# Kernel optimization log

Hardware: AMD Instinct MI355X
Metric: run time of the kernel (lower is better)

The kernel has to match this reference:

```python
import jax, jax.numpy as jnp
import numpy as np
from jax import lax

D, H, DH, F, K, L, N = 512, 8, 64, 2048, 31, 512, 16
EPS = 1e-5

def layer_norm(x, g, b):
    m = x.mean(-1, keepdims=True)
    v = ((x - m) ** 2).mean(-1, keepdims=True)
    return (x - m) / jnp.sqrt(v + EPS) * g + b

def swish(x):
    return x * jax.nn.sigmoid(x)

def ffn(x, w1, b1, w2, b2):
    return swish(x @ w1.T + b1) @ w2.T + b2

def rel_shift(x):
    # x: (N,H,T,2T-1) -> (N,H,T,T); out[...,i,j] = x[...,i, T-1-i+j]
    T = x.shape[2]
    rows = jnp.arange(T)[:, None]
    cols = (T - 1) - rows + jnp.arange(T)[None, :]
    return x[:, :, rows, cols]

def rel_attn(x, pos_emb, in_w, in_b, out_w, out_b, pos_w, bu, bv):
    Lq, Nb, E = x.shape
    qkv = x @ in_w.T + in_b  # (L,N,3E)
    q, k, v = jnp.split(qkv, 3, axis=-1)
    q = q.reshape(Lq, Nb, H, DH).transpose(1, 2, 0, 3)  # (N,H,L,DH)
    k = k.reshape(Lq, Nb, H, DH).transpose(1, 2, 0, 3)
    v = v.reshape(Lq, Nb, H, DH).transpose(1, 2, 0, 3)
    p = (pos_emb[0] @ pos_w.T).reshape(-1, H, DH).transpose(1, 0, 2)  # (H,2L-1,DH)
    scaling = DH ** -0.5
    q_u = q + bu[None, :, None, :]
    q_v = q + bv[None, :, None, :]
    matrix_ac = jnp.einsum('nhld,nhsd->nhls', q_u, k)        # (N,H,L,L)
    matrix_bd = jnp.einsum('nhld,hmd->nhlm', q_v, p)         # (N,H,L,2L-1)
    matrix_bd = rel_shift(matrix_bd)                         # (N,H,L,L)
    attn = jax.nn.softmax((matrix_ac + matrix_bd) * scaling, axis=-1)
    out = jnp.einsum('nhls,nhsd->nhld', attn, v)
    out = out.transpose(2, 0, 1, 3).reshape(Lq, Nb, E)
    return out @ out_w.T + out_b

def conv_module(x, pw1_w, pw1_b, dw_w, dw_b, g, b, mean, var, pw2_w, pw2_b):
    # x: (L,N,C) -> (N,C,L)
    y = x.transpose(1, 2, 0)
    y = jnp.einsum('ncl,oc->nol', y, pw1_w) + pw1_b[None, :, None]
    a, gate = jnp.split(y, 2, axis=1)
    y = a * jax.nn.sigmoid(gate)  # GLU over channel dim
    pad = (K - 1) // 2
    y = lax.conv_general_dilated(y, dw_w[:, None, :], (1,), [(pad, pad)],
                                 feature_group_count=D,
                                 dimension_numbers=('NCH', 'OIH', 'NCH'))
    y = y + dw_b[None, :, None]
    # BatchNorm1d in eval mode with running stats
    y = (y - mean[None, :, None]) / jnp.sqrt(var[None, :, None] + EPS)
    y = y * g[None, :, None] + b[None, :, None]
    y = swish(y)
    y = jnp.einsum('ncl,oc->nol', y, pw2_w) + pw2_b[None, :, None]
    return y.transpose(2, 0, 1)  # back to (L,N,C)

def setup_inputs() -> dict:
    key = jax.random.key(0)
    ks = iter(jax.random.split(key, 64))
    def nrm(shape, s=0.02):
        return jax.random.normal(next(ks), shape, dtype=jnp.float32) * s
    return {
        'src': jax.random.normal(next(ks), (L, N, D), dtype=jnp.float32),
        'pos_emb': jax.random.normal(next(ks), (1, 2 * L - 1, D), dtype=jnp.float32),
        'ffm_w1': nrm((F, D)), 'ffm_b1': jnp.zeros((F,), jnp.float32),
        'ffm_w2': nrm((D, F)), 'ffm_b2': jnp.zeros((D,), jnp.float32),
        'ff_w1': nrm((F, D)), 'ff_b1': jnp.zeros((F,), jnp.float32),
        'ff_w2': nrm((D, F)), 'ff_b2': jnp.zeros((D,), jnp.float32),
        'in_proj_w': nrm((3 * D, D)), 'in_proj_b': jnp.zeros((3 * D,), jnp.float32),
        'out_proj_w': nrm((D, D)), 'out_proj_b': jnp.zeros((D,), jnp.float32),
        'pos_w': nrm((D, D)),
        'pos_bias_u': nrm((H, DH)), 'pos_bias_v': nrm((H, DH)),
        'conv_pw1_w': nrm((2 * D, D)), 'conv_pw1_b': jnp.zeros((2 * D,), jnp.float32),
        'conv_dw_w': nrm((D, K)), 'conv_dw_b': jnp.zeros((D,), jnp.float32),
        'bn_gamma': jnp.ones((D,), jnp.float32), 'bn_beta': jnp.zeros((D,), jnp.float32),
        'bn_mean': jnp.zeros((D,), jnp.float32), 'bn_var': jnp.ones((D,), jnp.float32),
        'conv_pw2_w': nrm((D, D)), 'conv_pw2_b': jnp.zeros((D,), jnp.float32),
        'ln_ffm_g': jnp.ones((D,), jnp.float32), 'ln_ffm_b': jnp.zeros((D,), jnp.float32),
        'ln_mha_g': jnp.ones((D,), jnp.float32), 'ln_mha_b': jnp.zeros((D,), jnp.float32),
        'ln_conv_g': jnp.ones((D,), jnp.float32), 'ln_conv_b': jnp.zeros((D,), jnp.float32),
        'ln_ff_g': jnp.ones((D,), jnp.float32), 'ln_ff_b': jnp.zeros((D,), jnp.float32),
        'ln_final_g': jnp.ones((D,), jnp.float32), 'ln_final_b': jnp.zeros((D,), jnp.float32),
    }

def reference(src, pos_emb, ffm_w1, ffm_b1, ffm_w2, ffm_b2, ff_w1, ff_b1, ff_w2, ff_b2,
              in_proj_w, in_proj_b, out_proj_w, out_proj_b, pos_w, pos_bias_u, pos_bias_v,
              conv_pw1_w, conv_pw1_b, conv_dw_w, conv_dw_b, bn_gamma, bn_beta, bn_mean, bn_var,
              conv_pw2_w, conv_pw2_b, ln_ffm_g, ln_ffm_b, ln_mha_g, ln_mha_b, ln_conv_g, ln_conv_b,
              ln_ff_g, ln_ff_b, ln_final_g, ln_final_b):
    # pre-norm conformer block, ff_scale = 0.5, dropout omitted (eval)
    x = src
    x = x + 0.5 * ffn(layer_norm(x, ln_ffm_g, ln_ffm_b), ffm_w1, ffm_b1, ffm_w2, ffm_b2)
    x = x + rel_attn(layer_norm(x, ln_mha_g, ln_mha_b), pos_emb,
                     in_proj_w, in_proj_b, out_proj_w, out_proj_b,
                     pos_w, pos_bias_u, pos_bias_v)
    x = x + conv_module(layer_norm(x, ln_conv_g, ln_conv_b),
                        conv_pw1_w, conv_pw1_b, conv_dw_w, conv_dw_b,
                        bn_gamma, bn_beta, bn_mean, bn_var, conv_pw2_w, conv_pw2_b)
    x = x + 0.5 * ffn(layer_norm(x, ln_ff_g, ln_ff_b), ff_w1, ff_b1, ff_w2, ff_b2)
    return layer_norm(x, ln_final_g, ln_final_b)
```

## Files before the change

kernel.cpp:

```cpp
#include <hip/hip_runtime.h>
#include <cstdint>
#include <cstddef>

typedef unsigned short u16;
typedef __attribute__((ext_vector_type(4))) float f32x4;
typedef __attribute__((ext_vector_type(8))) short bf16x8;
typedef __attribute__((ext_vector_type(8))) unsigned short u16x8;

__device__ __forceinline__ float sigm(float x) { return 1.f / (1.f + __expf(-x)); }
__device__ __forceinline__ float bf2f(u16 u) {
    union { unsigned int i; float f; } c; c.i = ((unsigned int)u) << 16; return c.f;
}
__device__ __forceinline__ u16 f2bf(float f) {
    union { float f; unsigned int i; } c; c.f = f;
    unsigned int x = c.i;
    x += 0x7fffu + ((x >> 16) & 1u);
    return (u16)(x >> 16);
}


__global__ void castall_k(const float* __restrict__ s0, const float* __restrict__ s1,
                          const float* __restrict__ s2, const float* __restrict__ s3,
                          const float* __restrict__ s4, const float* __restrict__ s5,
                          const float* __restrict__ s6, const float* __restrict__ s7,
                          const float* __restrict__ s8, const float* __restrict__ s9,
                          u16* __restrict__ dst) {
    int i = blockIdx.x * 256 + threadIdx.x;
    if (i >= 6815232) return;
    const float* s; int off;
    if      (i < 1048576) { s = s0; off = 0; }
    else if (i < 2097152) { s = s1; off = 1048576; }
    else if (i < 3145728) { s = s2; off = 2097152; }
    else if (i < 4194304) { s = s3; off = 3145728; }
    else if (i < 4980736) { s = s4; off = 4194304; }
    else if (i < 5242880) { s = s5; off = 4980736; }
    else if (i < 5767168) { s = s6; off = 5242880; }
    else if (i < 6029312) { s = s7; off = 5767168; }
    else if (i < 6291456) { s = s8; off = 6029312; }
    else                  { s = s9; off = 6291456; }
    dst[i] = f2bf(s[i - off]);
}

template <bool OUTBF>
__global__ __launch_bounds__(256) void ln512_k(const float* __restrict__ x,
                                               const float* __restrict__ g,
                                               const float* __restrict__ b,
                                               void* __restrict__ outv) {
    int row = blockIdx.x * 4 + (threadIdx.x >> 6);
    int lane = threadIdx.x & 63;
    const float* xr = x + (size_t)row * 512 + lane * 8;
    float4 v0 = *(const float4*)(xr);
    float4 v1 = *(const float4*)(xr + 4);
    float va[8] = {v0.x, v0.y, v0.z, v0.w, v1.x, v1.y, v1.z, v1.w};
    float s = 0.f;
#pragma unroll
    for (int t = 0; t < 8; t++) s += va[t];
#pragma unroll
    for (int o = 32; o > 0; o >>= 1) s += __shfl_xor(s, o);
    float m = s * (1.0f / 512.0f);
    float q = 0.f;
#pragma unroll
    for (int t = 0; t < 8; t++) { float d = va[t] - m; q += d * d; }
#pragma unroll
    for (int o = 32; o > 0; o >>= 1) q += __shfl_xor(q, o);
    float inv = rsqrtf(q * (1.0f / 512.0f) + 1e-5f);
    int cb = lane * 8;
    if (OUTBF) {
        u16* o = (u16*)outv + (size_t)row * 512 + cb;
#pragma unroll
        for (int t = 0; t < 8; t++)
            o[t] = f2bf((va[t] - m) * inv * g[cb + t] + b[cb + t]);
    } else {
        float* o = (float*)outv + (size_t)row * 512 + cb;
#pragma unroll
        for (int t = 0; t < 8; t++)
            o[t] = (va[t] - m) * inv * g[cb + t] + b[cb + t];
    }
}

__global__ __launch_bounds__(512) void mgemm_k(
    const u16* __restrict__ A, const u16* __restrict__ B, const float* __restrict__ bias,
    const float* __restrict__ add, void* __restrict__ Cv,
    int M, int Nn, int Kk, float coef, int act, int outbf) {
    __shared__ u16 lA[2][4096];
    __shared__ u16 lB[2][4096];
    int tid = threadIdx.x;
    int half = tid >> 8;
    int t128 = tid & 255;
    int lane = tid & 63;
    int w = (tid >> 6) & 3;
    int wm = (w >> 1) * 64, wn = (w & 1) * 64;
    int m0 = blockIdx.x << 7, n0 = blockIdx.y << 7;
    int Kh = Kk >> 1;
    int kbase = half * Kh;

    f32x4 acc[4][4];
#pragma unroll
    for (int i = 0; i < 4; i++)
#pragma unroll
        for (int j = 0; j < 4; j++) acc[i][j] = (f32x4){0.f, 0.f, 0.f, 0.f};

    int srow = t128 >> 2;
    int scol = (t128 & 3) << 3;
    const u16* gA = A + (size_t)(m0 + srow) * Kk + kbase + scol;
    const u16* gB = B + (size_t)(n0 + srow) * Kk + kbase + scol;
    int lso = t128 * 8;

    int lra = wm * 32 + (lane & 15) * 32 + (lane >> 4) * 8;
    int lrb = wn * 32 + (lane & 15) * 32 + (lane >> 4) * 8;

    for (int k0 = 0; k0 < Kh; k0 += 32) {
        __builtin_amdgcn_global_load_lds(
            (const __attribute__((address_space(1))) void*)(gA + k0),
            (__attribute__((address_space(3))) void*)(lA[half] + lso), 16, 0, 0);
        __builtin_amdgcn_global_load_lds(
            (const __attribute__((address_space(1))) void*)(gA + (size_t)64 * Kk + k0),
            (__attribute__((address_space(3))) void*)(lA[half] + 2048 + lso), 16, 0, 0);
        __builtin_amdgcn_global_load_lds(
            (const __attribute__((address_space(1))) void*)(gB + k0),
            (__attribute__((address_space(3))) void*)(lB[half] + lso), 16, 0, 0);
        __builtin_amdgcn_global_load_lds(
            (const __attribute__((address_space(1))) void*)(gB + (size_t)64 * Kk + k0),
            (__attribute__((address_space(3))) void*)(lB[half] + 2048 + lso), 16, 0, 0);
        __syncthreads();
        bf16x8 af[4], bf[4];
#pragma unroll
        for (int t = 0; t < 4; t++) {
            af[t] = *(const bf16x8*)(lA[half] + lra + t * 512);
            bf[t] = *(const bf16x8*)(lB[half] + lrb + t * 512);
        }
#pragma unroll
        for (int i = 0; i < 4; i++)
#pragma unroll
            for (int j = 0; j < 4; j++)
                acc[i][j] = __builtin_amdgcn_mfma_f32_16x16x32_bf16(af[i], bf[j], acc[i][j], 0, 0, 0);
        __syncthreads();
    }

    float* red = (float*)lA;
#pragma unroll
    for (int rr = 0; rr < 4; rr++) {
        if (half == 1) {
#pragma unroll
            for (int j = 0; j < 4; j++)
                *(f32x4*)(red + ((w * 64 + lane) * 16 + j * 4)) = acc[rr][j];
        }
        __syncthreads();
        if (half == 0) {
#pragma unroll
            for (int j = 0; j < 4; j++) {
                f32x4 o = *(const f32x4*)(red + ((w * 64 + lane) * 16 + j * 4));
                acc[rr][j] += o;
            }
        }
        __syncthreads();
    }

    if (half == 0) {
        int rbase = (lane >> 4) * 4;
        int ncol = lane & 15;
#pragma unroll
        for (int i = 0; i < 4; i++) {
#pragma unroll
            for (int j = 0; j < 4; j++) {
                int n = n0 + wn + j * 16 + ncol;
                float bv = bias ? bias[n] : 0.f;
#pragma unroll
                for (int r = 0; r < 4; r++) {
                    int m = m0 + wm + i * 16 + rbase + r;
                    float c = acc[i][j][r] + bv;
                    if (act == 1) c *= sigm(c);
                    size_t o = (size_t)m * Nn + n;
                    if (add) c = add[o] + coef * c;
                    if (outbf) ((u16*)Cv)[o] = f2bf(c);
                    else ((float*)Cv)[o] = c;
                }
            }
        }
    }
}

__global__ __launch_bounds__(256) void posb_k(const u16* __restrict__ A,
                                              const u16* __restrict__ B,
                                              u16* __restrict__ Pbf) {
    __shared__ u16 lA[4096];
    __shared__ u16 lB[4096];
    const int Kk = 512;
    int tid = threadIdx.x;
    int lane = tid & 63, w = tid >> 6;
    int wm = (w >> 1) * 64, wn = (w & 1) * 64;
    int m0 = blockIdx.x << 7, n0 = blockIdx.y << 7;

    f32x4 acc[4][4];
#pragma unroll
    for (int i = 0; i < 4; i++)
#pragma unroll
        for (int j = 0; j < 4; j++) acc[i][j] = (f32x4){0.f, 0.f, 0.f, 0.f};

    int srow = tid >> 2;
    int scol = (tid & 3) << 3;
    int ar0 = m0 + srow;       if (ar0 > 1022) ar0 = 1022;
    int ar1 = m0 + 64 + srow;  if (ar1 > 1022) ar1 = 1022;
    const u16* gA0 = A + (size_t)ar0 * Kk + scol;
    const u16* gA1 = A + (size_t)ar1 * Kk + scol;
    const u16* gB = B + (size_t)(n0 + srow) * Kk + scol;
    int lso = tid * 8;
    int lra = wm * 32 + (lane & 15) * 32 + (lane >> 4) * 8;
    int lrb = wn * 32 + (lane & 15) * 32 + (lane >> 4) * 8;

    for (int k0 = 0; k0 < Kk; k0 += 32) {
        __builtin_amdgcn_global_load_lds(
            (const __attribute__((address_space(1))) void*)(gA0 + k0),
            (__attribute__((address_space(3))) void*)(lA + lso), 16, 0, 0);
        __builtin_amdgcn_global_load_lds(
            (const __attribute__((address_space(1))) void*)(gA1 + k0),
            (__attribute__((address_space(3))) void*)(lA + 2048 + lso), 16, 0, 0);
        __builtin_amdgcn_global_load_lds(
            (const __attribute__((address_space(1))) void*)(gB + k0),
            (__attribute__((address_space(3))) void*)(lB + lso), 16, 0, 0);
        __builtin_amdgcn_global_load_lds(
            (const __attribute__((address_space(1))) void*)(gB + (size_t)64 * Kk + k0),
            (__attribute__((address_space(3))) void*)(lB + 2048 + lso), 16, 0, 0);
        __syncthreads();
        bf16x8 af[4], bf[4];
#pragma unroll
        for (int t = 0; t < 4; t++) {
            af[t] = *(const bf16x8*)(lA + lra + t * 512);
            bf[t] = *(const bf16x8*)(lB + lrb + t * 512);
        }
#pragma unroll
        for (int i = 0; i < 4; i++)
#pragma unroll
            for (int j = 0; j < 4; j++)
                acc[i][j] = __builtin_amdgcn_mfma_f32_16x16x32_bf16(af[i], bf[j], acc[i][j], 0, 0, 0);
        __syncthreads();
    }

    int rbase = (lane >> 4) * 4;
    int ncol = lane & 15;
#pragma unroll
    for (int i = 0; i < 4; i++) {
#pragma unroll
        for (int j = 0; j < 4; j++) {
            int n = n0 + wn + j * 16 + ncol;
            int h = n >> 6, d = n & 63;
#pragma unroll
            for (int r = 0; r < 4; r++) {
                int m = m0 + wm + i * 16 + rbase + r;
                u16 val = (m < 1023) ? f2bf(acc[i][j][r]) : (u16)0;
                Pbf[(((size_t)(h * 1024 + m)) << 6) + d] = val;
            }
        }
    }
}

__global__ __launch_bounds__(256) void fattn_k(
    const u16* __restrict__ QU, const u16* __restrict__ QV,
    const u16* __restrict__ Kb, const u16* __restrict__ Pbf,
    const u16* __restrict__ VT, u16* __restrict__ ctx) {
    __shared__ u16 arr[19072];
    u16* sRect = arr;
    u16* sP = arr;
    u16* sCtx = arr + 16768;
    float* sRed = (float*)(arr + 18816);

    int tid = threadIdx.x;
    int lane = tid & 63, w = tid >> 6;
    int quad = lane >> 4, col = lane & 15;
    int nh = blockIdx.x, h = nh & 7, nb = nh >> 3;
    int m0 = blockIdx.y << 5;
    int nlo = 480 - m0;

    const u16* QVz = QV + ((size_t)nh << 15);
    const u16* QUz = QU + ((size_t)nh << 15);
    const u16* Kz  = Kb + ((size_t)nh << 15);
    const u16* Vz  = VT + ((size_t)nh << 15);
    const u16* Pb  = Pbf + ((size_t)h << 16);

    bf16x8 av[2][2];
#pragma unroll
    for (int ks = 0; ks < 2; ks++)
#pragma unroll
        for (int t = 0; t < 2; t++)
            av[ks][t] = *(const bf16x8*)(QVz + ((size_t)(m0 + t * 16 + col) << 6) + (ks << 5) + quad * 8);
#pragma unroll
    for (int idx = 0; idx < 9; idx++) {
        int nt = w + (idx << 2);
        if (nt < 34) {
            int crow = nt * 16 + col;
            const u16* pb = Pb + ((size_t)(nlo + crow) << 6) + quad * 8;
            f32x4 b0 = (f32x4){0.f, 0.f, 0.f, 0.f};
            f32x4 b1 = (f32x4){0.f, 0.f, 0.f, 0.f};
#pragma unroll
            for (int ks = 0; ks < 2; ks++) {
                bf16x8 bfr = *(const bf16x8*)(pb + (ks << 5));
                b0 = __builtin_amdgcn_mfma_f32_16x16x32_bf16(av[ks][0], bfr, b0, 0, 0, 0);
                b1 = __builtin_amdgcn_mfma_f32_16x16x32_bf16(av[ks][1], bfr, b1, 0, 0, 0);
            }
#pragma unroll
            for (int r = 0; r < 4; r++) {
                int ml0 = quad * 4 + r;
                int j0 = crow + ml0 - 31;
                if (j0 >= 0 && j0 < 512) sRect[ml0 * 524 + j0] = f2bf(b0[r]);
                int ml1 = ml0 + 16;
                int j1 = crow + ml1 - 31;
                if (j1 >= 0 && j1 < 512) sRect[ml1 * 524 + j1] = f2bf(b1[r]);
            }
        }
    }

    bf16x8 au[2][2];
#pragma unroll
    for (int ks = 0; ks < 2; ks++)
#pragma unroll
        for (int t = 0; t < 2; t++)
            au[ks][t] = *(const bf16x8*)(QUz + ((size_t)(m0 + t * 16 + col) << 6) + (ks << 5) + quad * 8);
    f32x4 ac[2][8];
#pragma unroll
    for (int t = 0; t < 2; t++)
#pragma unroll
        for (int jt = 0; jt < 8; jt++) ac[t][jt] = (f32x4){0.f, 0.f, 0.f, 0.f};
#pragma unroll
    for (int jt = 0; jt < 8; jt++) {
        const u16* kp = Kz + ((size_t)((w << 7) + jt * 16 + col) << 6) + quad * 8;
#pragma unroll
        for (int ks = 0; ks < 2; ks++) {
            bf16x8 bfr = *(const bf16x8*)(kp + (ks << 5));
            ac[0][jt] = __builtin_amdgcn_mfma_f32_16x16x32_bf16(au[ks][0], bfr, ac[0][jt], 0, 0, 0);
            ac[1][jt] = __builtin_amdgcn_mfma_f32_16x16x32_bf16(au[ks][1], bfr, ac[1][jt], 0, 0, 0);
        }
    }
    __syncthreads();

    float rmax[2][4];
#pragma unroll
    for (int t = 0; t < 2; t++)
#pragma unroll
        for (int r = 0; r < 4; r++) rmax[t][r] = -1e30f;
#pragma unroll
    for (int jt = 0; jt < 8; jt++) {
        int j = (w << 7) + jt * 16 + col;
#pragma unroll
        for (int t = 0; t < 2; t++)
#pragma unroll
            for (int r = 0; r < 4; r++) {
                int ml = t * 16 + quad * 4 + r;
                float v = (ac[t][jt][r] + bf2f(sRect[ml * 524 + j])) * 0.125f;
                ac[t][jt][r] = v;
                rmax[t][r] = fmaxf(rmax[t][r], v);
            }
    }
#pragma unroll
    for (int o = 1; o <= 8; o <<= 1)
#pragma unroll
        for (int t = 0; t < 2; t++)
#pragma unroll
            for (int r = 0; r < 4; r++) rmax[t][r] = fmaxf(rmax[t][r], __shfl_xor(rmax[t][r], o));
    if (col == 0)
#pragma unroll
        for (int t = 0; t < 2; t++)
#pragma unroll
            for (int r = 0; r < 4; r++) sRed[(t * 16 + quad * 4 + r) * 4 + w] = rmax[t][r];
    __syncthreads();
    float gmax[2][4], psum[2][4];
#pragma unroll
    for (int t = 0; t < 2; t++)
#pragma unroll
        for (int r = 0; r < 4; r++) {
            int ml = t * 16 + quad * 4 + r;
            gmax[t][r] = fmaxf(fmaxf(sRed[ml * 4 + 0], sRed[ml * 4 + 1]),
                               fmaxf(sRed[ml * 4 + 2], sRed[ml * 4 + 3]));
            psum[t][r] = 0.f;
        }
    __syncthreads();
#pragma unroll
    for (int jt = 0; jt < 8; jt++)
#pragma unroll
        for (int t = 0; t < 2; t++)
#pragma unroll
            for (int r = 0; r < 4; r++) {
                float e = __expf(ac[t][jt][r] - gmax[t][r]);
                ac[t][jt][r] = e;
                psum[t][r] += e;
            }
#pragma unroll
    for (int o = 1; o <= 8; o <<= 1)
#pragma unroll
        for (int t = 0; t < 2; t++)
#pragma unroll
            for (int r = 0; r < 4; r++) psum[t][r] += __shfl_xor(psum[t][r], o);
    if (col == 0)
#pragma unroll
        for (int t = 0; t < 2; t++)
#pragma unroll
            for (int r = 0; r < 4; r++) sRed[(t * 16 + quad * 4 + r) * 4 + w] = psum[t][r];
    __syncthreads();
    float rinv[2][4];
#pragma unroll
    for (int t = 0; t < 2; t++)
#pragma unroll
        for (int r = 0; r < 4; r++) {
            int ml = t * 16 + quad * 4 + r;
            rinv[t][r] = 1.f / (sRed[ml * 4 + 0] + sRed[ml * 4 + 1] + sRed[ml * 4 + 2] + sRed[ml * 4 + 3]);
        }

#pragma unroll
    for (int jt = 0; jt < 8; jt++) {
        int j = (w << 7) + jt * 16 + col;
#pragma unroll
        for (int t = 0; t < 2; t++)
#pragma unroll
            for (int r = 0; r < 4; r++)
                sP[(t * 16 + quad * 4 + r) * 520 + j] = f2bf(ac[t][jt][r] * rinv[t][r]);
    }
    __syncthreads();

    f32x4 cacc[2];
    cacc[0] = (f32x4){0.f, 0.f, 0.f, 0.f};
    cacc[1] = (f32x4){0.f, 0.f, 0.f, 0.f};
    {
        const u16* vp = Vz + ((size_t)((w << 4) + col) << 9) + quad * 8;
#pragma unroll
        for (int kc = 0; kc < 2; kc++)
#pragma unroll
            for (int s2 = 0; s2 < 8; s2++) {
                int ko = (kc << 8) + (s2 << 5);
                bf16x8 a0 = *(const bf16x8*)(sP + col * 520 + ko + quad * 8);
                bf16x8 a1 = *(const bf16x8*)(sP + (col + 16) * 520 + ko + quad * 8);
                bf16x8 bfr = *(const bf16x8*)(vp + ko);
                cacc[0] = __builtin_amdgcn_mfma_f32_16x16x32_bf16(a0, bfr, cacc[0], 0, 0, 0);
                cacc[1] = __builtin_amdgcn_mfma_f32_16x16x32_bf16(a1, bfr, cacc[1], 0, 0, 0);
            }
    }

#pragma unroll
    for (int t = 0; t < 2; t++)
#pragma unroll
        for (int r = 0; r < 4; r++)
            sCtx[(t * 16 + quad * 4 + r) * 64 + (w << 4) + col] = f2bf(cacc[t][r]);
    __syncthreads();
    {
        int row = tid >> 3, seg = tid & 7;
        u16* dst = ctx + (((size_t)((m0 + row) * 16 + nb)) << 9) + (h << 6) + seg * 8;
        *(uint4*)dst = *(const uint4*)(sCtx + row * 64 + seg * 8);
    }
}

__global__ __launch_bounds__(256) void repack_k(const u16* __restrict__ qkv,
                                                const float* __restrict__ bu,
                                                const float* __restrict__ bv,
                                                u16* __restrict__ QU, u16* __restrict__ QV,
                                                u16* __restrict__ Kb, u16* __restrict__ VT) {
    __shared__ u16 sV[64 * 72];
    int nh = blockIdx.x, h = nh & 7, n = nh >> 3;
    int l0 = blockIdx.y << 6;
    int tid = threadIdx.x;
    int d8 = (tid & 7) << 3;
    float bub[8], bvb[8];
#pragma unroll
    for (int e = 0; e < 8; e++) {
        bub[e] = bu[h * 64 + d8 + e];
        bvb[e] = bv[h * 64 + d8 + e];
    }
#pragma unroll
    for (int rep = 0; rep < 2; rep++) {
        int ll = (tid >> 3) + rep * 32;
        int l = l0 + ll;
        size_t base = (size_t)(l * 16 + n) * 1536 + h * 64 + d8;
        u16x8 q = *(const u16x8*)(qkv + base);
        u16x8 k = *(const u16x8*)(qkv + base + 512);
        u16x8 v = *(const u16x8*)(qkv + base + 1024);
        u16x8 qu, qv;
#pragma unroll
        for (int e = 0; e < 8; e++) {
            float qf = bf2f(q[e]);
            qu[e] = f2bf(qf + bub[e]);
            qv[e] = f2bf(qf + bvb[e]);
        }
        size_t o = ((size_t)nh * 512 + l) * 64 + d8;
        *(u16x8*)(QU + o) = qu;
        *(u16x8*)(QV + o) = qv;
        *(u16x8*)(Kb + o) = k;
        *(u16x8*)(sV + ll * 72 + d8) = v;
    }
    __syncthreads();
    int d = tid >> 2, ls = (tid & 3) << 4;
    u16 tmp[16];
#pragma unroll
    for (int e = 0; e < 16; e++) tmp[e] = sV[(ls + e) * 72 + d];
    u16* dst = VT + ((size_t)nh * 64 + d) * 512 + l0 + ls;
    *(u16x8*)(dst) = *(const u16x8*)(tmp);
    *(u16x8*)(dst + 8) = *(const u16x8*)(tmp + 8);
}

__global__ void glu_k(const u16* __restrict__ pw1o, u16* __restrict__ g) {
    int e = blockIdx.x * 256 + threadIdx.x;
    int t = e >> 9, c = e & 511;
    float a = bf2f(pw1o[(size_t)t * 1024 + c]);
    float ga = bf2f(pw1o[(size_t)t * 1024 + 512 + c]);
    g[e] = f2bf(a * sigm(ga));
}

__global__ __launch_bounds__(256) void dwconv_k(
    const u16* __restrict__ g, const float* __restrict__ w, const float* __restrict__ wb,
    const float* __restrict__ bng, const float* __restrict__ bnb, const float* __restrict__ bnm,
    const float* __restrict__ bnv, u16* __restrict__ out) {
    int idx = blockIdx.x * 256 + threadIdx.x;
    int c = idx & 511;
    int t = idx >> 9;
    int n = t & 15, l0 = (t >> 4) << 4;
    float win[46];
#pragma unroll
    for (int q = 0; q < 46; q++) {
        int ll = l0 - 15 + q;
        win[q] = (ll >= 0 && ll < 512) ? bf2f(g[((size_t)(ll * 16 + n) << 9) + c]) : 0.f;
    }
    float wgt[31];
#pragma unroll
    for (int k = 0; k < 31; k++) wgt[k] = w[c * 31 + k];
    float ivg = rsqrtf(bnv[c] + 1e-5f) * bng[c];
    float mc = bnm[c], bc = bnb[c], wbc = wb[c];
#pragma unroll
    for (int r = 0; r < 16; r++) {
        float acc = 0.f;
#pragma unroll
        for (int k = 0; k < 31; k++) acc += wgt[k] * win[r + k];
        acc += wbc;
        float y = (acc - mc) * ivg + bc;
        y = y * sigm(y);
        out[((size_t)((l0 + r) * 16 + n) << 9) + c] = f2bf(y);
    }
}

extern "C" void kernel_launch(void* const* d_in, const int* in_sizes, int n_in,
                              void* d_out, int out_size, void* d_ws, size_t ws_size,
                              hipStream_t stream) {
    const float* src      = (const float*)d_in[0];
    const float* pos_emb  = (const float*)d_in[1];
    const float* ffm_w1   = (const float*)d_in[2];
    const float* ffm_b1   = (const float*)d_in[3];
    const float* ffm_w2   = (const float*)d_in[4];
    const float* ffm_b2   = (const float*)d_in[5];
    const float* ff_w1    = (const float*)d_in[6];
    const float* ff_b1    = (const float*)d_in[7];
    const float* ff_w2    = (const float*)d_in[8];
    const float* ff_b2    = (const float*)d_in[9];
    const float* in_w     = (const float*)d_in[10];
    const float* in_b     = (const float*)d_in[11];
    const float* out_w    = (const float*)d_in[12];
    const float* out_b    = (const float*)d_in[13];
    const float* pos_w    = (const float*)d_in[14];
    const float* bu       = (const float*)d_in[15];
    const float* bv       = (const float*)d_in[16];
    const float* pw1_w    = (const float*)d_in[17];
    const float* pw1_b    = (const float*)d_in[18];
    const float* dw_w     = (const float*)d_in[19];
    const float* dw_b     = (const float*)d_in[20];
    const float* bng      = (const float*)d_in[21];
    const float* bnb      = (const float*)d_in[22];
    const float* bnm      = (const float*)d_in[23];
    const float* bnv      = (const float*)d_in[24];
    const float* pw2_w    = (const float*)d_in[25];
    const float* pw2_b    = (const float*)d_in[26];
    const float* ln_ffm_g = (const float*)d_in[27];
    const float* ln_ffm_b = (const float*)d_in[28];
    const float* ln_mha_g = (const float*)d_in[29];
    const float* ln_mha_b = (const float*)d_in[30];
    const float* ln_cv_g  = (const float*)d_in[31];
    const float* ln_cv_b  = (const float*)d_in[32];
    const float* ln_ff_g  = (const float*)d_in[33];
    const float* ln_ff_b  = (const float*)d_in[34];
    const float* ln_fin_g = (const float*)d_in[35];
    const float* ln_fin_b = (const float*)d_in[36];
    (void)in_sizes; (void)n_in; (void)out_size; (void)ws_size;

    const size_t MEG = 1048576;
    u16* U = (u16*)d_ws;
    float* xA = (float*)U;
    u16* Pbf = U;
    float* xB = (float*)(U + 8 * MEG);
    u16* LNB = U + 16 * MEG;
    u16* BIG = U + 20 * MEG;
    u16* QU = U + 36 * MEG;
    u16* QV = U + 40 * MEG;
    u16* Kb = U + 44 * MEG;
    u16* VT = U + 48 * MEG;
    u16* WB = U + 52 * MEG;
    u16* w_ffm1 = WB;
    u16* w_ffm2 = WB + 1 * MEG;
    u16* w_ff1  = WB + 2 * MEG;
    u16* w_ff2  = WB + 3 * MEG;
    u16* w_in   = WB + 4 * MEG;
    u16* w_out  = WB + 4 * MEG + 786432;
    u16* w_pw1  = WB + 5 * MEG;
    u16* w_pw2  = WB + 5 * MEG + 524288;
    u16* w_pos  = WB + 6029312;
    u16* w_pe   = WB + 6291456;
    u16* CTX = LNB;
    u16* GLU = QU;
    u16* CACT = QV;

    castall_k<<<26622, 256, 0, stream>>>(ffm_w1, ffm_w2, ff_w1, ff_w2, in_w, out_w,
                                         pw1_w, pw2_w, pos_w, pos_emb, WB);

    ln512_k<true><<<2048, 256, 0, stream>>>(src, ln_ffm_g, ln_ffm_b, LNB);
    mgemm_k<<<dim3(64, 16), 512, 0, stream>>>(LNB, w_ffm1, ffm_b1, nullptr, BIG,
                                              8192, 2048, 512, 0.f, 1, 1);
    mgemm_k<<<dim3(64, 4), 512, 0, stream>>>(BIG, w_ffm2, ffm_b2, src, xB,
                                             8192, 512, 2048, 0.5f, 0, 0);

    ln512_k<true><<<2048, 256, 0, stream>>>(xB, ln_mha_g, ln_mha_b, LNB);
    posb_k<<<dim3(8, 4), 256, 0, stream>>>(w_pe, w_pos, Pbf);
    mgemm_k<<<dim3(64, 12), 512, 0, stream>>>(LNB, w_in, in_b, nullptr, BIG,
                                              8192, 1536, 512, 0.f, 0, 1);
    repack_k<<<dim3(128, 8), 256, 0, stream>>>(BIG, bu, bv, QU, QV, Kb, VT);
    fattn_k<<<dim3(128, 16), 256, 0, stream>>>(QU, QV, Kb, Pbf, VT, CTX);
    mgemm_k<<<dim3(64, 4), 512, 0, stream>>>(CTX, w_out, out_b, xB, xA,
                                             8192, 512, 512, 1.f, 0, 0);

    ln512_k<true><<<2048, 256, 0, stream>>>(xA, ln_cv_g, ln_cv_b, LNB);
    mgemm_k<<<dim3(64, 8), 512, 0, stream>>>(LNB, w_pw1, pw1_b, nullptr, BIG,
                                             8192, 1024, 512, 0.f, 0, 1);
    glu_k<<<16384, 256, 0, stream>>>(BIG, GLU);
    dwconv_k<<<1024, 256, 0, stream>>>(GLU, dw_w, dw_b, bng, bnb, bnm, bnv, CACT);
    mgemm_k<<<dim3(64, 4), 512, 0, stream>>>(CACT, w_pw2, pw2_b, xA, xB,
                                             8192, 512, 512, 1.f, 0, 0);

    ln512_k<true><<<2048, 256, 0, stream>>>(xB, ln_ff_g, ln_ff_b, LNB);
    mgemm_k<<<dim3(64, 16), 512, 0, stream>>>(LNB, w_ff1, ff_b1, nullptr, BIG,
                                              8192, 2048, 512, 0.f, 1, 1);
    mgemm_k<<<dim3(64, 4), 512, 0, stream>>>(BIG, w_ff2, ff_b2, xB, xA,
                                             8192, 512, 2048, 0.5f, 0, 0);

    ln512_k<false><<<2048, 256, 0, stream>>>(xA, ln_fin_g, ln_fin_b, (float*)d_out);
}
```

Measured before the change: 620.1 us.

## Replace split-K half-blocks with double-buffered single-pass GEMM pipeline

The GEMM kernel previously split K across two 256-thread halves of a 512-thread block and reduced the partial sums through LDS. It now uses 256 threads over the full K with two LDS buffers, issuing the next tile's async global-to-LDS load while MFMAs run on the current tile. This removes the cross-half reduction and its barriers and overlaps memory with compute. The trade-off is fewer waves per block and twice as many K iterations per wave.

```diff
diff --git a/kernel.cpp b/kernel.cpp
--- a/kernel.cpp
+++ b/kernel.cpp
@@ -78,21 +78,17 @@
     }
 }
 
-__global__ __launch_bounds__(512) void mgemm_k(
+__global__ __launch_bounds__(256) void mgemm_k(
     const u16* __restrict__ A, const u16* __restrict__ B, const float* __restrict__ bias,
     const float* __restrict__ add, void* __restrict__ Cv,
     int M, int Nn, int Kk, float coef, int act, int outbf) {
     __shared__ u16 lA[2][4096];
     __shared__ u16 lB[2][4096];
     int tid = threadIdx.x;
-    int half = tid >> 8;
-    int t128 = tid & 255;
     int lane = tid & 63;
-    int w = (tid >> 6) & 3;
+    int w = tid >> 6;
     int wm = (w >> 1) * 64, wn = (w & 1) * 64;
     int m0 = blockIdx.x << 7, n0 = blockIdx.y << 7;
-    int Kh = Kk >> 1;
-    int kbase = half * Kh;
 
     f32x4 acc[4][4];
 #pragma unroll
@@ -100,81 +96,69 @@
 #pragma unroll
         for (int j = 0; j < 4; j++) acc[i][j] = (f32x4){0.f, 0.f, 0.f, 0.f};
 
-    int srow = t128 >> 2;
-    int scol = (t128 & 3) << 3;
-    const u16* gA = A + (size_t)(m0 + srow) * Kk + kbase + scol;
-    const u16* gB = B + (size_t)(n0 + srow) * Kk + kbase + scol;
-    int lso = t128 * 8;
-
+    int srow = tid >> 2;
+    int scol = (tid & 3) << 3;
+    const u16* gA = A + (size_t)(m0 + srow) * Kk + scol;
+    const u16* gB = B + (size_t)(n0 + srow) * Kk + scol;
+    int lso = tid * 8;
     int lra = wm * 32 + (lane & 15) * 32 + (lane >> 4) * 8;
     int lrb = wn * 32 + (lane & 15) * 32 + (lane >> 4) * 8;
 
-    for (int k0 = 0; k0 < Kh; k0 += 32) {
+    auto STAGE = [&](int buf, int k0) {
         __builtin_amdgcn_global_load_lds(
             (const __attribute__((address_space(1))) void*)(gA + k0),
-            (__attribute__((address_space(3))) void*)(lA[half] + lso), 16, 0, 0);
+            (__attribute__((address_space(3))) void*)(lA[buf] + lso), 16, 0, 0);
         __builtin_amdgcn_global_load_lds(
             (const __attribute__((address_space(1))) void*)(gA + (size_t)64 * Kk + k0),
-            (__attribute__((address_space(3))) void*)(lA[half] + 2048 + lso), 16, 0, 0);
+            (__attribute__((address_space(3))) void*)(lA[buf] + 2048 + lso), 16, 0, 0);
         __builtin_amdgcn_global_load_lds(
             (const __attribute__((address_space(1))) void*)(gB + k0),
-            (__attribute__((address_space(3))) void*)(lB[half] + lso), 16, 0, 0);
+            (__attribute__((address_space(3))) void*)(lB[buf] + lso), 16, 0, 0);
         __builtin_amdgcn_global_load_lds(
             (const __attribute__((address_space(1))) void*)(gB + (size_t)64 * Kk + k0),
-            (__attribute__((address_space(3))) void*)(lB[half] + 2048 + lso), 16, 0, 0);
-        __syncthreads();
+            (__attribute__((address_space(3))) void*)(lB[buf] + 2048 + lso), 16, 0, 0);
+    };
+    auto COMP = [&](int buf) {
         bf16x8 af[4], bf[4];
 #pragma unroll
         for (int t = 0; t < 4; t++) {
-            af[t] = *(const bf16x8*)(lA[half] + lra + t * 512);
-            bf[t] = *(const bf16x8*)(lB[half] + lrb + t * 512);
+            af[t] = *(const bf16x8*)(lA[buf] + lra + t * 512);
+            bf[t] = *(const bf16x8*)(lB[buf] + lrb + t * 512);
         }
 #pragma unroll
         for (int i = 0; i < 4; i++)
 #pragma unroll
             for (int j = 0; j < 4; j++)
                 acc[i][j] = __builtin_amdgcn_mfma_f32_16x16x32_bf16(af[i], bf[j], acc[i][j], 0, 0, 0);
+    };
+
+    int nk = Kk >> 5;
+    STAGE(0, 0);
+    __syncthreads();
+    for (int kt = 1; kt < nk; kt++) {
+        STAGE(kt & 1, kt << 5);
+        COMP((kt - 1) & 1);
         __syncthreads();
     }
-
-    float* red = (float*)lA;
-#pragma unroll
-    for (int rr = 0; rr < 4; rr++) {
-        if (half == 1) {
-#pragma unroll
-            for (int j = 0; j < 4; j++)
-                *(f32x4*)(red + ((w * 64 + lane) * 16 + j * 4)) = acc[rr][j];
-        }
-        __syncthreads();
-        if (half == 0) {
-#pragma unroll
-            for (int j = 0; j < 4; j++) {
-                f32x4 o = *(const f32x4*)(red + ((w * 64 + lane) * 16 + j * 4));
-                acc[rr][j] += o;
-            }
-        }
-        __syncthreads();
-    }
-
-    if (half == 0) {
-        int rbase = (lane >> 4) * 4;
-        int ncol = lane & 15;
-#pragma unroll
-        for (int i = 0; i < 4; i++) {
-#pragma unroll
-            for (int j = 0; j < 4; j++) {
-                int n = n0 + wn + j * 16 + ncol;
-                float bv = bias ? bias[n] : 0.f;
-#pragma unroll
-                for (int r = 0; r < 4; r++) {
-                    int m = m0 + wm + i * 16 + rbase + r;
-                    float c = acc[i][j][r] + bv;
-                    if (act == 1) c *= sigm(c);
-                    size_t o = (size_t)m * Nn + n;
-                    if (add) c = add[o] + coef * c;
-                    if (outbf) ((u16*)Cv)[o] = f2bf(c);
-                    else ((float*)Cv)[o] = c;
-                }
+    COMP((nk - 1) & 1);
+
+    int rbase = (lane >> 4) * 4;
+    int ncol = lane & 15;
+#pragma unroll
+    for (int i = 0; i < 4; i++) {
+#pragma unroll
+        for (int j = 0; j < 4; j++) {
+            int n = n0 + wn + j * 16 + ncol;
+            float bv = bias ? bias[n] : 0.f;
+#pragma unroll
+            for (int r = 0; r < 4; r++) {
+                int m = m0 + wm + i * 16 + rbase + r;
+                float c = acc[i][j][r] + bv;
+                if (act == 1) c *= sigm(c);
+                size_t o = (size_t)m * Nn + n;
+                if (add) c = add[o] + coef * c;
+                if (outbf) ((u16*)Cv)[o] = f2bf(c);
+                else ((float*)Cv)[o] = c;
             }
         }
     }
@@ -604,32 +588,32 @@
                                          pw1_w, pw2_w, pos_w, pos_emb, WB);
 
     ln512_k<true><<<2048, 256, 0, stream>>>(src, ln_ffm_g, ln_ffm_b, LNB);
-    mgemm_k<<<dim3(64, 16), 512, 0, stream>>>(LNB, w_ffm1, ffm_b1, nullptr, BIG,
+    mgemm_k<<<dim3(64, 16), 256, 0, stream>>>(LNB, w_ffm1, ffm_b1, nullptr, BIG,
                                               8192, 2048, 512, 0.f, 1, 1);
-    mgemm_k<<<dim3(64, 4), 512, 0, stream>>>(BIG, w_ffm2, ffm_b2, src, xB,
+    mgemm_k<<<dim3(64, 4), 256, 0, stream>>>(BIG, w_ffm2, ffm_b2, src, xB,
                                              8192, 512, 2048, 0.5f, 0, 0);
 
     ln512_k<true><<<2048, 256, 0, stream>>>(xB, ln_mha_g, ln_mha_b, LNB);
     posb_k<<<dim3(8, 4), 256, 0, stream>>>(w_pe, w_pos, Pbf);
-    mgemm_k<<<dim3(64, 12), 512, 0, stream>>>(LNB, w_in, in_b, nullptr, BIG,
+    mgemm_k<<<dim3(64, 12), 256, 0, stream>>>(LNB, w_in, in_b, nullptr, BIG,
                                               8192, 1536, 512, 0.f, 0, 1);
     repack_k<<<dim3(128, 8), 256, 0, stream>>>(BIG, bu, bv, QU, QV, Kb, VT);
     fattn_k<<<dim3(128, 16), 256, 0, stream>>>(QU, QV, Kb, Pbf, VT, CTX);
-    mgemm_k<<<dim3(64, 4), 512, 0, stream>>>(CTX, w_out, out_b, xB, xA,
+    mgemm_k<<<dim3(64, 4), 256, 0, stream>>>(CTX, w_out, out_b, xB, xA,
                                              8192, 512, 512, 1.f, 0, 0);
 
     ln512_k<true><<<2048, 256, 0, stream>>>(xA, ln_cv_g, ln_cv_b, LNB);
-    mgemm_k<<<dim3(64, 8), 512, 0, stream>>>(LNB, w_pw1, pw1_b, nullptr, BIG,
+    mgemm_k<<<dim3(64, 8), 256, 0, stream>>>(LNB, w_pw1, pw1_b, nullptr, BIG,
                                              8192, 1024, 512, 0.f, 0, 1);
     glu_k<<<16384, 256, 0, stream>>>(BIG, GLU);
     dwconv_k<<<1024, 256, 0, stream>>>(GLU, dw_w, dw_b, bng, bnb, bnm, bnv, CACT);
-    mgemm_k<<<dim3(64, 4), 512, 0, stream>>>(CACT, w_pw2, pw2_b, xA, xB,
+    mgemm_k<<<dim3(64, 4), 256, 0, stream>>>(CACT, w_pw2, pw2_b, xA, xB,
                                              8192, 512, 512, 1.f, 0, 0);
 
     ln512_k<true><<<2048, 256, 0, stream>>>(xB, ln_ff_g, ln_ff_b, LNB);
-    mgemm_k<<<dim3(64, 16), 512, 0, stream>>>(LNB, w_ff1, ff_b1, nullptr, BIG,
+    mgemm_k<<<dim3(64, 16), 256, 0, stream>>>(LNB, w_ff1, ff_b1, nullptr, BIG,
                                               8192, 2048, 512, 0.f, 1, 1);
-    mgemm_k<<<dim3(64, 4), 512, 0, stream>>>(BIG, w_ff2, ff_b2, xB, xA,
+    mgemm_k<<<dim3(64, 4), 256, 0, stream>>>(BIG, w_ff2, ff_b2, xB, xA,
                                              8192, 512, 2048, 0.5f, 0, 0);
 
     ln512_k<false><<<2048, 256, 0, stream>>>(xA, ln_fin_g, ln_fin_b, (float*)d_out);
```

After: 607.5 us. 1.02x faster.
